# Optimization experiments

Hardware: AMD Instinct MI355X
Metric: run time of the kernel (lower is better)

## Reference

```python
import jax, jax.numpy as jnp
import numpy as np

D_MODEL = 1024

def setup_inputs() -> dict:
    key = jax.random.key(0)
    ks = jax.random.split(key, 7)
    x = jax.random.normal(ks[0], (4, 2048, D_MODEL), dtype=jnp.float32)
    s = 1.0 / np.sqrt(D_MODEL)
    Wq = jax.random.uniform(ks[1], (D_MODEL, D_MODEL), jnp.float32, -s, s)
    bq = jax.random.uniform(ks[2], (D_MODEL,), jnp.float32, -s, s)
    Wk = jax.random.uniform(ks[3], (D_MODEL, D_MODEL), jnp.float32, -s, s)
    bk = jax.random.uniform(ks[4], (D_MODEL,), jnp.float32, -s, s)
    Wv = jax.random.uniform(ks[5], (D_MODEL, D_MODEL), jnp.float32, -s, s)
    bv = jax.random.uniform(ks[6], (D_MODEL,), jnp.float32, -s, s)
    return {"x": x, "Wq": Wq, "bq": bq, "Wk": Wk, "bk": bk, "Wv": Wv, "bv": bv}

def reference(x, Wq, bq, Wk, bk, Wv, bv):
    # x: [B, S, D]; Linear weights stored torch-style [out, in] -> y = x @ W.T + b
    B, S, D = x.shape
    q = jnp.einsum('bsd,ed->bse', x, Wq) + bq
    k = jnp.einsum('bsd,ed->bse', x, Wk) + bk
    v = jnp.einsum('bsd,ed->bse', x, Wv) + bv
    scores = jnp.einsum('bqd,bkd->bqk', q, k) / jnp.sqrt(jnp.float32(D))
    causal = jnp.tril(jnp.ones((S, S), dtype=bool))  # True = allowed
    scores = jnp.where(causal[None], scores, -jnp.inf)
    probs = jax.nn.softmax(scores, axis=-1)
    return jnp.einsum('bqk,bkd->bqd', probs, v)
```

## Files before the change

### kernel.cpp

```cpp
#include <hip/hip_runtime.h>
#include <hip/hip_bf16.h>
#include <stdint.h>

using bf16 = __hip_bfloat16;
typedef __bf16 bf16x8 __attribute__((ext_vector_type(8)));
typedef float  f32x4  __attribute__((ext_vector_type(4)));
typedef long   i64;
typedef unsigned char u8;

#define AS1 __attribute__((address_space(1)))
#define AS3 __attribute__((address_space(3)))

__device__ __forceinline__ void async_cp16(const void* g, void* l) {
    __builtin_amdgcn_global_load_lds((const AS1 void*)g, (AS3 void*)l, 16, 0, 0);
}

__device__ __forceinline__ unsigned pk8_lo(float a, float b, unsigned old) {
    return __builtin_amdgcn_cvt_pk_fp8_f32(a, b, old, false);
}

#define BARRIER() asm volatile("s_barrier" ::: "memory")
#define WAITV(N)  asm volatile("s_waitcnt vmcnt(" #N ")" ::: "memory")

__device__ __forceinline__ void ld_bfrag(const char* lB, int wn, int quad, int r16,
                                         bf16x8 (&bfr)[4][2])
{
#pragma unroll
    for (int nt = 0; nt < 4; nt++) {
        int row = wn + nt * 16 + r16;
#pragma unroll
        for (int kk = 0; kk < 2; kk++) {
            int slot = (kk * 4 + quad) ^ (row & 7);
            bfr[nt][kk] = *(const bf16x8*)(lB + row * 128 + slot * 16);
        }
    }
}

__device__ __forceinline__ void ld_afrag(const char* lA, int wm, int quad, int r16, int q,
                                         bf16x8 (&af)[2][2])
{
#pragma unroll
    for (int t = 0; t < 2; t++) {
        int row = wm + (q * 2 + t) * 16 + r16;
#pragma unroll
        for (int kk = 0; kk < 2; kk++) {
            int slot = (kk * 4 + quad) ^ (row & 7);
            af[t][kk] = *(const bf16x8*)(lA + row * 128 + slot * 16);
        }
    }
}

__device__ __forceinline__ void mfma_quad(int q, bf16x8 (&af)[2][2], bf16x8 (&bfr)[4][2],
                                          f32x4 (&acc)[8][4])
{
    __builtin_amdgcn_s_setprio(1);
#pragma unroll
    for (int mt = 0; mt < 2; mt++)
#pragma unroll
        for (int nt = 0; nt < 4; nt++)
#pragma unroll
            for (int kk = 0; kk < 2; kk++)
                acc[q * 2 + mt][nt] = __builtin_amdgcn_mfma_f32_16x16x32_bf16(
                    af[mt][kk], bfr[nt][kk], acc[q * 2 + mt][nt], 0, 0, 0);
    __builtin_amdgcn_s_setprio(0);
}

__global__ __launch_bounds__(512, 2) void gemm_qkv(
    const bf16* __restrict__ xb,
    const bf16* __restrict__ Wqb, const bf16* __restrict__ Wkb, const bf16* __restrict__ Wvb,
    const float* __restrict__ bq, const float* __restrict__ bk, const float* __restrict__ bv,
    u8* __restrict__ Qq, u8* __restrict__ Kq, bf16* __restrict__ Vt)
{
    extern __shared__ char smem[];
    const int bn = blockIdx.x, bm = blockIdx.y;
    const int seg = bn >> 2, bn_loc = bn & 3;
    const bf16*  W    = seg == 0 ? Wqb : (seg == 1 ? Wkb : Wvb);
    const float* bias = seg == 0 ? bq  : (seg == 1 ? bk  : bv);

    const int tid  = threadIdx.x;
    const int wave = tid >> 6, lane = tid & 63;
    const int wm = (wave >> 2) * 128, wn = (wave & 3) * 64;
    const int quad = lane >> 4, r16 = lane & 15;

    char* A0 = smem;
    char* A1 = smem + 32768;
    char* B0 = smem + 65536;
    char* B1 = smem + 98304;

    const bf16* Ab = xb + (long)bm * 256 * 1024;
    const bf16* Bb = W  + (long)bn_loc * 256 * 1024;

    const int rl  = lane >> 3;
    const int cbg = (lane & 7) ^ rl;
    const bf16* gA = Ab + (long)(wave * 32 + rl) * 1024 + cbg * 8;
    const bf16* gB = Bb + (long)(wave * 32 + rl) * 1024 + cbg * 8;
    const int woff = wave * 4096;

    auto stage = [&](char* dst, const bf16* src, int k0, int c) {
        async_cp16(src + (long)c * 8192 + k0, dst + woff + c * 1024);
    };

    f32x4 acc[8][4];
    const f32x4 zero = {0.f, 0.f, 0.f, 0.f};
#pragma unroll
    for (int i = 0; i < 8; i++)
#pragma unroll
        for (int j = 0; j < 4; j++) acc[i][j] = zero;

#pragma unroll
    for (int c = 0; c < 4; c++) stage(B0, gB, 0, c);
#pragma unroll
    for (int c = 0; c < 4; c++) stage(A0, gA, 0, c);
#pragma unroll
    for (int c = 0; c < 4; c++) stage(B1, gB, 64, c);
    stage(A1, gA, 64, 0); stage(A1, gA, 64, 1);
    WAITV(6);
    BARRIER();

    bf16x8 bfr[4][2], af[2][2];
#pragma unroll 1
    for (int i = 0; i < 8; ++i) {
        const int kO  = i * 128 + 64;
        const int kE2 = i * 128 + 128;
        const int kO2 = i * 128 + 192;
        const bool pre = (i < 7);

        ld_bfrag(B0, wn, quad, r16, bfr);
        ld_afrag(A0, wm, quad, r16, 0, af);
        stage(A1, gA, kO, 2); stage(A1, gA, kO, 3);
        BARRIER();
        mfma_quad(0, af, bfr, acc);
        BARRIER();
        ld_afrag(A0, wm, quad, r16, 1, af);
        if (pre) { stage(B0, gB, kE2, 0); stage(B0, gB, kE2, 1); }
        BARRIER();
        mfma_quad(1, af, bfr, acc);
        BARRIER();
        ld_afrag(A0, wm, quad, r16, 2, af);
        if (pre) { stage(B0, gB, kE2, 2); stage(B0, gB, kE2, 3); }
        BARRIER();
        mfma_quad(2, af, bfr, acc);
        BARRIER();
        ld_afrag(A0, wm, quad, r16, 3, af);
        if (pre) { stage(A0, gA, kE2, 0); stage(A0, gA, kE2, 1); WAITV(6); }
        else     { WAITV(0); }
        BARRIER();
        mfma_quad(3, af, bfr, acc);
        BARRIER();
        ld_bfrag(B1, wn, quad, r16, bfr);
        ld_afrag(A1, wm, quad, r16, 0, af);
        if (pre) { stage(A0, gA, kE2, 2); stage(A0, gA, kE2, 3); }
        BARRIER();
        mfma_quad(0, af, bfr, acc);
        BARRIER();
        ld_afrag(A1, wm, quad, r16, 1, af);
        if (pre) { stage(B1, gB, kO2, 0); stage(B1, gB, kO2, 1); }
        BARRIER();
        mfma_quad(1, af, bfr, acc);
        BARRIER();
        ld_afrag(A1, wm, quad, r16, 2, af);
        if (pre) { stage(B1, gB, kO2, 2); stage(B1, gB, kO2, 3); }
        BARRIER();
        mfma_quad(2, af, bfr, acc);
        BARRIER();
        ld_afrag(A1, wm, quad, r16, 3, af);
        if (pre) { stage(A1, gA, kO2, 0); stage(A1, gA, kO2, 1); WAITV(6); }
        BARRIER();
        mfma_quad(3, af, bfr, acc);
        BARRIER();
    }

    if (seg < 2) {
        u8* O = seg == 0 ? Qq : Kq;
#pragma unroll
        for (int mt = 0; mt < 8; mt++) {
#pragma unroll
            for (int nt = 0; nt < 4; nt++) {
                int col = bn_loc * 256 + wn + nt * 16 + r16;
                float badd = bias[col];
#pragma unroll
                for (int rg = 0; rg < 4; rg++) {
                    long token = (long)bm * 256 + wm + mt * 16 + quad * 4 + rg;
                    float v = acc[mt][nt][rg] + badd;
                    O[token * 1024 + col] = (u8)(pk8_lo(v, v, 0u) & 0xFF);
                }
            }
        }
    } else {
#pragma unroll
        for (int mt = 0; mt < 8; mt++) {
#pragma unroll
            for (int nt = 0; nt < 4; nt++) {
                int col = bn_loc * 256 + wn + nt * 16 + r16;
                float badd = bias[col];
                long token0 = (long)bm * 256 + wm + mt * 16 + quad * 4;
                union { ushort4 u; bf16 h[4]; } o;
#pragma unroll
                for (int rg = 0; rg < 4; rg++)
                    o.h[rg] = __float2bfloat16(acc[mt][nt][rg] + badd);
                *(ushort4*)&Vt[(long)col * 8192 + token0] = o.u;
            }
        }
    }
}

__global__ __launch_bounds__(256, 2) void gemm_scores(
    const u8* __restrict__ Qq, const u8* __restrict__ Kq,
    bf16* __restrict__ P, float* __restrict__ spart)
{
    const int t = blockIdx.x, bz = blockIdx.z;
    int bm = (int)((sqrtf(8.f * t + 1.f) - 1.f) * 0.5f);
    while ((bm + 1) * (bm + 2) / 2 <= t) bm++;
    while (bm * (bm + 1) / 2 > t) bm--;
    const int bn = t - bm * (bm + 1) / 2;
    const bool diag = (bn == bm);

    __shared__ u8 sA[2][128 * 128];
    __shared__ u8 sB[2][128 * 128];

    const int tid  = threadIdx.x;
    const int wave = tid >> 6, lane = tid & 63;
    const int wm = (wave >> 1) * 64, wn = (wave & 1) * 64;
    const int quad = lane >> 4, r16 = lane & 15;
    const int whalf = wave & 1;

    const u8* Ab = Qq + (long)bz * 2048 * 1024 + (long)bm * 128 * 1024;
    const u8* Bb = Kq + (long)bz * 2048 * 1024 + (long)bn * 128 * 1024;

    const int rl = lane >> 3;
    const int cb = (lane & 7) ^ rl;
    const u8* gA = Ab + (long)(wave * 32 + rl) * 1024 + cb * 16;
    const u8* gB = Bb + (long)(wave * 32 + rl) * 1024 + cb * 16;

    f32x4 acc[4][4];
    const f32x4 zero = {0.f, 0.f, 0.f, 0.f};
#pragma unroll
    for (int i = 0; i < 4; i++)
#pragma unroll
        for (int j = 0; j < 4; j++) acc[i][j] = zero;

    for (int it = 0; it < 4; ++it) {
        const int k0 = it * 256;
#pragma unroll
        for (int s = 0; s < 2; s++) {
            u8* lA = sA[s] + wave * 32 * 128;
            u8* lB = sB[s] + wave * 32 * 128;
#pragma unroll
            for (int c = 0; c < 4; c++) {
                async_cp16(gA + (long)c * 8 * 1024 + k0 + s * 128, lA + c * 1024);
                async_cp16(gB + (long)c * 8 * 1024 + k0 + s * 128, lB + c * 1024);
            }
        }
        __syncthreads();
#pragma unroll
        for (int s = 0; s < 2; s++) {
#pragma unroll
            for (int kk = 0; kk < 4; kk++) {
                const int g  = kk * 2 + (quad >> 1);
                const int hb = (quad & 1) * 8;
                i64 av[4], bv[4];
#pragma unroll
                for (int t2 = 0; t2 < 4; t2++) {
                    int row  = wm + t2 * 16 + r16;
                    int slot = g ^ (row & 7);
                    av[t2] = *(const i64*)(sA[s] + row * 128 + slot * 16 + hb);
                }
#pragma unroll
                for (int t2 = 0; t2 < 4; t2++) {
                    int row  = wn + t2 * 16 + r16;
                    int slot = g ^ (row & 7);
                    bv[t2] = *(const i64*)(sB[s] + row * 128 + slot * 16 + hb);
                }
#pragma unroll
                for (int mt = 0; mt < 4; mt++)
#pragma unroll
                    for (int nt = 0; nt < 4; nt++)
                        acc[mt][nt] = __builtin_amdgcn_mfma_f32_16x16x32_fp8_fp8(
                            av[mt], bv[nt], acc[mt][nt], 0, 0, 0);
            }
        }
        __syncthreads();
    }

    bf16* Pb = P + (long)bz * 2048 * 2048 + (long)bm * 128 * 2048 + bn * 128;
    float rowsum[4][4];
#pragma unroll
    for (int mt = 0; mt < 4; mt++)
#pragma unroll
        for (int rg = 0; rg < 4; rg++) rowsum[mt][rg] = 0.f;

#pragma unroll
    for (int mt = 0; mt < 4; mt++) {
#pragma unroll
        for (int nt = 0; nt < 4; nt++) {
            int rcol = wn + nt * 16 + r16;
#pragma unroll
            for (int rg = 0; rg < 4; rg++) {
                int rrow = wm + mt * 16 + quad * 4 + rg;
                float e = (diag && rcol > rrow)
                            ? 0.f : __expf(acc[mt][nt][rg] * 0.03125f);
                Pb[(long)rrow * 2048 + rcol] = __float2bfloat16(e);
                rowsum[mt][rg] += e;
            }
        }
    }
#pragma unroll
    for (int off = 1; off < 16; off <<= 1)
#pragma unroll
        for (int mt = 0; mt < 4; mt++)
#pragma unroll
            for (int rg = 0; rg < 4; rg++)
                rowsum[mt][rg] += __shfl_xor(rowsum[mt][rg], off);

    float* red = (float*)sA;
    if (r16 == 0) {
#pragma unroll
        for (int mt = 0; mt < 4; mt++)
#pragma unroll
            for (int rg = 0; rg < 4; rg++)
                red[whalf * 128 + wm + mt * 16 + quad * 4 + rg] = rowsum[mt][rg];
    }
    __syncthreads();
    if (tid < 128)
        spart[((long)bz * 16 + bn) * 2048 + bm * 128 + tid] = red[tid] + red[128 + tid];
}

__global__ __launch_bounds__(256, 2) void gemm_pv(
    const bf16* __restrict__ P, const bf16* __restrict__ Vt,
    const float* __restrict__ spart, float* __restrict__ out)
{
    const int bn = blockIdx.x, by = blockIdx.y, bz = blockIdx.z;
    const int bm = (bz < 2) ? (15 - by) : by;
    const int nb = bm + 1;

    __shared__ bf16 sA[2][128 * 64];
    __shared__ bf16 sB[2][128 * 64];
    __shared__ float invl[128];

    const int tid  = threadIdx.x;
    const int wave = tid >> 6, lane = tid & 63;
    const int wm = (wave >> 1) * 64, wn = (wave & 1) * 64;
    const int quad = lane >> 4, r16 = lane & 15;

    if (tid < 128) {
        long base = (long)bz * 16 * 2048 + (long)bm * 128 + tid;
        float l = 0.f;
        for (int j = 0; j < nb; j++) l += spart[base + j * 2048];
        invl[tid] = 1.f / l;
    }

    const bf16* Ab = P  + (long)bz * 2048 * 2048 + (long)bm * 128 * 2048;
    const bf16* Bb = Vt + (long)bz * 2048 + (long)bn * 128 * 8192;

    const int rl = lane >> 3;
    const int cb = (lane & 7) ^ rl;
    const bf16* gA = Ab + (long)(wave * 32 + rl) * 2048 + cb * 8;
    const bf16* gB = Bb + (long)(wave * 32 + rl) * 8192 + cb * 8;

    f32x4 acc[4][4];
    const f32x4 zero = {0.f, 0.f, 0.f, 0.f};
#pragma unroll
    for (int i = 0; i < 4; i++)
#pragma unroll
        for (int j = 0; j < 4; j++) acc[i][j] = zero;

    for (int it = 0; it < nb; ++it) {
        const int k0 = it * 128;
#pragma unroll
        for (int s = 0; s < 2; s++) {
            char* lA = (char*)sA[s] + wave * 32 * 128;
            char* lB = (char*)sB[s] + wave * 32 * 128;
#pragma unroll
            for (int c = 0; c < 4; c++) {
                async_cp16(gA + (long)c * 8 * 2048 + k0 + s * 64, lA + c * 1024);
                async_cp16(gB + (long)c * 8 * 8192 + k0 + s * 64, lB + c * 1024);
            }
        }
        __syncthreads();
#pragma unroll
        for (int s = 0; s < 2; s++) {
#pragma unroll
            for (int kk = 0; kk < 2; kk++) {
                bf16x8 af[4], bfr[4];
#pragma unroll
                for (int t = 0; t < 4; t++) {
                    int row  = wm + t * 16 + r16;
                    int slot = (kk * 4 + quad) ^ (row & 7);
                    af[t] = *(const bf16x8*)((const char*)sA[s] + row * 128 + slot * 16);
                }
#pragma unroll
                for (int t = 0; t < 4; t++) {
                    int row  = wn + t * 16 + r16;
                    int slot = (kk * 4 + quad) ^ (row & 7);
                    bfr[t] = *(const bf16x8*)((const char*)sB[s] + row * 128 + slot * 16);
                }
#pragma unroll
                for (int mt = 0; mt < 4; mt++)
#pragma unroll
                    for (int nt = 0; nt < 4; nt++)
                        acc[mt][nt] = __builtin_amdgcn_mfma_f32_16x16x32_bf16(
                            af[mt], bfr[nt], acc[mt][nt], 0, 0, 0);
            }
        }
        __syncthreads();
    }

    float* Ob = out + (long)bz * 2048 * 1024 + (long)bm * 128 * 1024 + bn * 128;
#pragma unroll
    for (int mt = 0; mt < 4; mt++) {
#pragma unroll
        for (int nt = 0; nt < 4; nt++) {
            int rcol = wn + nt * 16 + r16;
#pragma unroll
            for (int rg = 0; rg < 4; rg++) {
                int rrow = wm + mt * 16 + quad * 4 + rg;
                Ob[(long)rrow * 1024 + rcol] = acc[mt][nt][rg] * invl[rrow];
            }
        }
    }
}

__global__ __launch_bounds__(256) void cvt_all(
    const float* __restrict__ x,
    const float* __restrict__ Wq, const float* __restrict__ Wk, const float* __restrict__ Wv,
    bf16* __restrict__ xb, bf16* __restrict__ dq, bf16* __restrict__ dk, bf16* __restrict__ dv)
{
    int b = blockIdx.x;
    const float* s; bf16* d; long off;
    if (b < 8192) { s = x; d = xb; off = (long)b * 1024; }
    else {
        int w = (b - 8192) >> 10, lb = (b - 8192) & 1023;
        s = w == 0 ? Wq : (w == 1 ? Wk : Wv);
        d = w == 0 ? dq : (w == 1 ? dk : dv);
        off = (long)lb * 1024;
    }
    long i = off + threadIdx.x * 4;
    float4 v = *(const float4*)(s + i);
    union { ushort4 u; bf16 h[4]; } o;
    o.h[0] = __float2bfloat16(v.x);
    o.h[1] = __float2bfloat16(v.y);
    o.h[2] = __float2bfloat16(v.z);
    o.h[3] = __float2bfloat16(v.w);
    *(ushort4*)(d + i) = o.u;
}

extern "C" void kernel_launch(void* const* d_in, const int* in_sizes, int n_in,
                              void* d_out, int out_size, void* d_ws, size_t ws_size,
                              hipStream_t stream)
{
    (void)in_sizes; (void)n_in; (void)out_size; (void)ws_size;
    const float* x  = (const float*)d_in[0];
    const float* Wq = (const float*)d_in[1];
    const float* bq = (const float*)d_in[2];
    const float* Wk = (const float*)d_in[3];
    const float* bk = (const float*)d_in[4];
    const float* Wv = (const float*)d_in[5];
    const float* bv = (const float*)d_in[6];
    float* out = (float*)d_out;

    char* ws = (char*)d_ws;
    bf16* xb  = (bf16*)ws;  ws += (long)8192 * 1024 * 2;
    bf16* Wqb = (bf16*)ws;  ws += (long)1024 * 1024 * 2;
    bf16* Wkb = (bf16*)ws;  ws += (long)1024 * 1024 * 2;
    bf16* Wvb = (bf16*)ws;  ws += (long)1024 * 1024 * 2;
    u8*  Qq   = (u8*)ws;    ws += (long)8192 * 1024;
    u8*  Kq   = (u8*)ws;    ws += (long)8192 * 1024;
    bf16* Vt  = (bf16*)ws;  ws += (long)8192 * 1024 * 2;
    bf16* P   = (bf16*)ws;  ws += (long)4 * 2048 * 2048 * 2;
    float* spart = (float*)ws; ws += (long)4 * 16 * 2048 * 4;

    static bool attr_set = false;
    if (!attr_set) {
        hipFuncSetAttribute(reinterpret_cast<const void*>(gemm_qkv),
                            hipFuncAttributeMaxDynamicSharedMemorySize, 131072);
        attr_set = true;
    }

    cvt_all<<<8192 + 3072, 256, 0, stream>>>(x, Wq, Wk, Wv, xb, Wqb, Wkb, Wvb);

    gemm_qkv<<<dim3(12, 32), 512, 131072, stream>>>(
        xb, Wqb, Wkb, Wvb, bq, bk, bv, Qq, Kq, Vt);

    gemm_scores<<<dim3(136, 1, 4), 256, 0, stream>>>(Qq, Kq, P, spart);

    gemm_pv<<<dim3(8, 16, 4), 256, 0, stream>>>(P, Vt, spart, out);
}
```

Baseline: 225.6 us.

## Rebalance QKV GEMM prefetch schedule and add XCD-aware block remapping

The QKV GEMM replaces inline-asm barriers with builtin s_barrier plus sched_barrier fences and spreads the async global-to-LDS stages more evenly across the eight MFMA phases. The prologue no longer preloads half of A1, and the vmcnt waits are retuned to match. The scores and PV kernels remap linear block IDs so that blocks sharing the same Q/P rows and batch land on the same XCD, aiming to improve L2 reuse. The risks are less prefetch slack in the GEMM and a modulo-based swizzle that must exactly match the grid size.

```diff
diff --git a/kernel.cpp b/kernel.cpp
--- a/kernel.cpp
+++ b/kernel.cpp
@@ -19,8 +19,10 @@
     return __builtin_amdgcn_cvt_pk_fp8_f32(a, b, old, false);
 }
 
-#define BARRIER() asm volatile("s_barrier" ::: "memory")
-#define WAITV(N)  asm volatile("s_waitcnt vmcnt(" #N ")" ::: "memory")
+#define SBAR()   do { __builtin_amdgcn_s_barrier(); \
+                      __builtin_amdgcn_sched_barrier(0); } while (0)
+#define WAITV(N) do { asm volatile("s_waitcnt vmcnt(" #N ")"); \
+                      __builtin_amdgcn_sched_barrier(0); } while (0)
 
 __device__ __forceinline__ void ld_bfrag(const char* lB, int wn, int quad, int r16,
                                          bf16x8 (&bfr)[4][2])
@@ -61,7 +63,7 @@
 #pragma unroll
             for (int kk = 0; kk < 2; kk++)
                 acc[q * 2 + mt][nt] = __builtin_amdgcn_mfma_f32_16x16x32_bf16(
-                    af[mt][kk], bfr[nt][kk], acc[q * 2 + mt][nt], 0, 0, 0);
+                    af[mt][kk], bfr[nt][kk], acc[q * 2 + mt][kk == 0 ? nt : nt], 0, 0, 0);
     __builtin_amdgcn_s_setprio(0);
 }
 
@@ -113,9 +115,8 @@
     for (int c = 0; c < 4; c++) stage(A0, gA, 0, c);
 #pragma unroll
     for (int c = 0; c < 4; c++) stage(B1, gB, 64, c);
-    stage(A1, gA, 64, 0); stage(A1, gA, 64, 1);
-    WAITV(6);
-    BARRIER();
+    WAITV(4);
+    SBAR();
 
     bf16x8 bfr[4][2], af[2][2];
 #pragma unroll 1
@@ -127,47 +128,47 @@
 
         ld_bfrag(B0, wn, quad, r16, bfr);
         ld_afrag(A0, wm, quad, r16, 0, af);
+        stage(A1, gA, kO, 0); stage(A1, gA, kO, 1);
+        SBAR();
+        mfma_quad(0, af, bfr, acc);
+        SBAR();
+        ld_afrag(A0, wm, quad, r16, 1, af);
         stage(A1, gA, kO, 2); stage(A1, gA, kO, 3);
-        BARRIER();
-        mfma_quad(0, af, bfr, acc);
-        BARRIER();
-        ld_afrag(A0, wm, quad, r16, 1, af);
+        SBAR();
+        mfma_quad(1, af, bfr, acc);
+        SBAR();
+        ld_afrag(A0, wm, quad, r16, 2, af);
         if (pre) { stage(B0, gB, kE2, 0); stage(B0, gB, kE2, 1); }
-        BARRIER();
-        mfma_quad(1, af, bfr, acc);
-        BARRIER();
-        ld_afrag(A0, wm, quad, r16, 2, af);
-        if (pre) { stage(B0, gB, kE2, 2); stage(B0, gB, kE2, 3); }
-        BARRIER();
+        SBAR();
         mfma_quad(2, af, bfr, acc);
-        BARRIER();
+        SBAR();
         ld_afrag(A0, wm, quad, r16, 3, af);
-        if (pre) { stage(A0, gA, kE2, 0); stage(A0, gA, kE2, 1); WAITV(6); }
+        if (pre) { stage(B0, gB, kE2, 2); stage(B0, gB, kE2, 3); WAITV(4); }
         else     { WAITV(0); }
-        BARRIER();
+        SBAR();
         mfma_quad(3, af, bfr, acc);
-        BARRIER();
+        SBAR();
         ld_bfrag(B1, wn, quad, r16, bfr);
         ld_afrag(A1, wm, quad, r16, 0, af);
+        if (pre) { stage(A0, gA, kE2, 0); stage(A0, gA, kE2, 1); }
+        SBAR();
+        mfma_quad(0, af, bfr, acc);
+        SBAR();
+        ld_afrag(A1, wm, quad, r16, 1, af);
         if (pre) { stage(A0, gA, kE2, 2); stage(A0, gA, kE2, 3); }
-        BARRIER();
-        mfma_quad(0, af, bfr, acc);
-        BARRIER();
-        ld_afrag(A1, wm, quad, r16, 1, af);
+        SBAR();
+        mfma_quad(1, af, bfr, acc);
+        SBAR();
+        ld_afrag(A1, wm, quad, r16, 2, af);
         if (pre) { stage(B1, gB, kO2, 0); stage(B1, gB, kO2, 1); }
-        BARRIER();
-        mfma_quad(1, af, bfr, acc);
-        BARRIER();
-        ld_afrag(A1, wm, quad, r16, 2, af);
-        if (pre) { stage(B1, gB, kO2, 2); stage(B1, gB, kO2, 3); }
-        BARRIER();
+        SBAR();
         mfma_quad(2, af, bfr, acc);
-        BARRIER();
+        SBAR();
         ld_afrag(A1, wm, quad, r16, 3, af);
-        if (pre) { stage(A1, gA, kO2, 0); stage(A1, gA, kO2, 1); WAITV(6); }
-        BARRIER();
+        if (pre) { stage(B1, gB, kO2, 2); stage(B1, gB, kO2, 3); WAITV(4); }
+        SBAR();
         mfma_quad(3, af, bfr, acc);
-        BARRIER();
+        SBAR();
     }
 
     if (seg < 2) {
@@ -208,7 +209,9 @@
     const u8* __restrict__ Qq, const u8* __restrict__ Kq,
     bf16* __restrict__ P, float* __restrict__ spart)
 {
-    const int t = blockIdx.x, bz = blockIdx.z;
+    const int lin = blockIdx.x + 136 * blockIdx.z;
+    const int ntg = (lin & 7) * 68 + (lin >> 3);
+    const int t = ntg % 136, bz = ntg / 136;
     int bm = (int)((sqrtf(8.f * t + 1.f) - 1.f) * 0.5f);
     while ((bm + 1) * (bm + 2) / 2 <= t) bm++;
     while (bm * (bm + 1) / 2 > t) bm--;
@@ -329,9 +332,14 @@
     const bf16* __restrict__ P, const bf16* __restrict__ Vt,
     const float* __restrict__ spart, float* __restrict__ out)
 {
-    const int bn = blockIdx.x, by = blockIdx.y, bz = blockIdx.z;
-    const int bm = (bz < 2) ? (15 - by) : by;
-    const int nb = bm + 1;
+    const int lin = blockIdx.x + 8 * blockIdx.y + 128 * blockIdx.z;
+    const int xcd = lin & 7;
+    const int m   = lin >> 3;
+    const int bn  = m & 7;
+    const int g   = xcd + 8 * (m >> 3);
+    const int by  = g & 15, bz = g >> 4;
+    const int bm  = (bz < 2) ? (15 - by) : by;
+    const int nb  = bm + 1;
 
     __shared__ bf16 sA[2][128 * 64];
     __shared__ bf16 sB[2][128 * 64];
```

New measurement: 220.2 us. -2.4%, faster.
